# Kernel tuning notes

Hardware: AMD Instinct MI355X
Metric: run time of the kernel (lower is better)

The kernel has to match this reference:

```python
import jax, jax.numpy as jnp
import numpy as np

N_NODES = 100000
N_EDGES = 1600000
IN_C, HID, OUT_C = 128, 128, 64
BN_EPS = 1e-5


def gcn_conv(x, W, b, src, dst):
    # PyG GCNConv(normalize=False): linear first, then sum-aggregate over edges
    m = x @ W                                   # [N, out_dim]
    agg = jax.ops.segment_sum(m[src], dst, num_segments=N_NODES)  # scatter-add by dst
    return agg + b


def batch_norm(h, gamma, beta):
    mu = jnp.mean(h, axis=0)
    var = jnp.var(h, axis=0)
    return (h - mu) * jax.lax.rsqrt(var + BN_EPS) * gamma + beta


def setup_inputs() -> dict:
    key = jax.random.key(0)
    ks = jax.random.split(key, 8)
    x = jax.random.normal(ks[0], (N_NODES, IN_C), dtype=jnp.float32)
    edge_src = jax.random.randint(ks[1], (N_EDGES,), 0, N_NODES, dtype=jnp.int32)
    edge_dst = jnp.sort(jax.random.randint(ks[2], (N_EDGES,), 0, N_NODES, dtype=jnp.int32))
    def glorot(k, shape):
        lim = float(np.sqrt(6.0 / (shape[0] + shape[1])))
        return jax.random.uniform(k, shape, jnp.float32, -lim, lim)
    return {
        "x": x, "edge_src": edge_src, "edge_dst": edge_dst,
        "W0": glorot(ks[3], (IN_C, HID)), "b0": jnp.zeros((HID,), jnp.float32),
        "W1": glorot(ks[4], (HID, HID)), "b1": jnp.zeros((HID,), jnp.float32),
        "W2": glorot(ks[5], (HID, OUT_C)), "b2": jnp.zeros((OUT_C,), jnp.float32),
        "g0": jnp.ones((HID,), jnp.float32), "be0": jnp.zeros((HID,), jnp.float32),
        "g1": jnp.ones((HID,), jnp.float32), "be1": jnp.zeros((HID,), jnp.float32),
    }


def reference(x, edge_src, edge_dst, W0, b0, W1, b1, W2, b2, g0, be0, g1, be1):
    # layer 0: conv -> BN -> residual (dims match: 128==128) -> ReLU (dropout p=0)
    h = gcn_conv(x, W0, b0, edge_src, edge_dst)
    h = batch_norm(h, g0, be0)
    h = h + x  # residual, in_channels == hidden_channels
    x1 = jax.nn.relu(h)
    # layer 1
    h = gcn_conv(x1, W1, b1, edge_src, edge_dst)
    h = batch_norm(h, g1, be1)
    h = h + x1
    x2 = jax.nn.relu(h)
    # final layer: conv only
    return gcn_conv(x2, W2, b2, edge_src, edge_dst)
```

## Files before the change

kernel.cpp:

```cpp
#include <hip/hip_runtime.h>

#define BN_EPS 1e-5f

typedef __attribute__((ext_vector_type(8))) short bf16x8;
typedef __attribute__((ext_vector_type(4))) float f32x4;

__device__ __forceinline__ short f2bf(float f) {
    union { float f; unsigned u; } v; v.f = f;
    unsigned r = (v.u + 0x7fffu + ((v.u >> 16) & 1u)) >> 16;
    return (short)r;
}
__device__ __forceinline__ float bflo(unsigned d) {
    union { unsigned u; float f; } v; v.u = d << 16; return v.f;
}
__device__ __forceinline__ float bfhi(unsigned d) {
    union { unsigned u; float f; } v; v.u = d & 0xffff0000u; return v.f;
}

__global__ __launch_bounds__(256) void build_off_k(const int* __restrict__ dst,
                                                   int* __restrict__ off, int E, int N) {
    int i = blockIdx.x * 256 + threadIdx.x;
    if (i > E) return;
    int cur  = (i < E) ? dst[i] : N;
    int prev = (i == 0) ? -1 : dst[i - 1];
    for (int n = prev + 1; n <= cur; ++n) off[n] = i;
}

__global__ void zero_k(float* p, int n) {
    int i = blockIdx.x * blockDim.x + threadIdx.x;
    if (i < n) p[i] = 0.f;
}

__global__ __launch_bounds__(256) void wtrans_k(const float* __restrict__ W,
                                                short* __restrict__ Wt, int K, int C) {
    int i = blockIdx.x * 256 + threadIdx.x;
    if (i >= K * C) return;
    int c = i / K, k = i % K;
    Wt[i] = f2bf(W[k * C + c]);
}

template <int OUTC, int MODE>
__global__ __launch_bounds__(256) void mgemm_k(const float* __restrict__ X,
                                               const short* __restrict__ Wt,
                                               short* __restrict__ M,
                                               const float* __restrict__ ss,
                                               const void* __restrict__ Rp,
                                               short* __restrict__ X1, int N) {
    constexpr int NR = OUTC / 16;
    __shared__ short sW[OUTC][136];

    const int tid = threadIdx.x;
    for (int q = tid; q < OUTC * 16; q += 256) {
        int r = q >> 4, s = q & 15;
        *(int4*)&sW[r][s * 8] = ((const int4*)Wt)[q];
    }
    __syncthreads();

    const int wave = tid >> 6, lane = tid & 63;
    const int lr = lane & 15, lg = lane >> 4;
    const int row0 = blockIdx.x * 128 + wave * 32;

    f32x4 acc[2][NR];
    #pragma unroll
    for (int m = 0; m < 2; ++m)
        #pragma unroll
        for (int n = 0; n < NR; ++n) acc[m][n] = (f32x4){0.f, 0.f, 0.f, 0.f};

    #pragma unroll
    for (int kk = 0; kk < 4; ++kk) {
        bf16x8 a[2];
        const int ch0 = kk * 32 + lg * 8;
        #pragma unroll
        for (int m = 0; m < 2; ++m) {
            int row = row0 + m * 16 + lr;
            float v[8] = {0.f, 0.f, 0.f, 0.f, 0.f, 0.f, 0.f, 0.f};
            if (row < N) {
                const float4* p = (const float4*)&X[(size_t)row * 128 + ch0];
                float4 h0 = p[0], h1 = p[1];
                v[0] = h0.x; v[1] = h0.y; v[2] = h0.z; v[3] = h0.w;
                v[4] = h1.x; v[5] = h1.y; v[6] = h1.z; v[7] = h1.w;
                if constexpr (MODE != 0) {
                    float4 sc0 = *(const float4*)&ss[ch0];
                    float4 sc1 = *(const float4*)&ss[ch0 + 4];
                    float4 sh0 = *(const float4*)&ss[128 + ch0];
                    float4 sh1 = *(const float4*)&ss[128 + ch0 + 4];
                    float sc[8] = {sc0.x, sc0.y, sc0.z, sc0.w, sc1.x, sc1.y, sc1.z, sc1.w};
                    float sh[8] = {sh0.x, sh0.y, sh0.z, sh0.w, sh1.x, sh1.y, sh1.z, sh1.w};
                    float r[8];
                    if constexpr (MODE == 1) {
                        const float4* rp = (const float4*)((const float*)Rp + (size_t)row * 128 + ch0);
                        float4 r0 = rp[0], r1 = rp[1];
                        r[0] = r0.x; r[1] = r0.y; r[2] = r0.z; r[3] = r0.w;
                        r[4] = r1.x; r[5] = r1.y; r[6] = r1.z; r[7] = r1.w;
                    } else {
                        int4 rb = *(const int4*)((const short*)Rp + (size_t)row * 128 + ch0);
                        r[0] = bflo(rb.x); r[1] = bfhi(rb.x);
                        r[2] = bflo(rb.y); r[3] = bfhi(rb.y);
                        r[4] = bflo(rb.z); r[5] = bfhi(rb.z);
                        r[6] = bflo(rb.w); r[7] = bfhi(rb.w);
                    }
                    #pragma unroll
                    for (int k = 0; k < 8; ++k)
                        v[k] = fmaxf(fmaf(v[k], sc[k], sh[k]) + r[k], 0.f);
                }
            }
            #pragma unroll
            for (int k = 0; k < 8; ++k) a[m][k] = f2bf(v[k]);
            if constexpr (MODE == 1) {
                if (row < N) *(bf16x8*)&X1[(size_t)row * 128 + ch0] = a[m];
            }
        }
        #pragma unroll
        for (int n = 0; n < NR; ++n) {
            bf16x8 b = *(const bf16x8*)&sW[n * 16 + lr][kk * 32 + lg * 8];
            acc[0][n] = __builtin_amdgcn_mfma_f32_16x16x32_bf16(a[0], b, acc[0][n], 0, 0, 0);
            acc[1][n] = __builtin_amdgcn_mfma_f32_16x16x32_bf16(a[1], b, acc[1][n], 0, 0, 0);
        }
    }

    #pragma unroll
    for (int m = 0; m < 2; ++m)
        #pragma unroll
        for (int r = 0; r < 4; ++r) {
            int row = row0 + m * 16 + lg * 4 + r;
            if (row < N) {
                #pragma unroll
                for (int n = 0; n < NR; ++n)
                    M[(size_t)row * OUTC + n * 16 + lr] = f2bf(acc[m][n][r]);
            }
        }
}

template <int C, bool STATS>
__global__ __launch_bounds__(256) void agg_k(const short* __restrict__ M,
                                             const int* __restrict__ src,
                                             const int* __restrict__ off,
                                             const float* __restrict__ bias,
                                             float* __restrict__ H,
                                             float* __restrict__ stats, int N) {
    constexpr int T = C / 8;
    constexpr int G = 64 / T;
    const int wave = threadIdx.x >> 6, lane = threadIdx.x & 63;
    const int g = lane / T, t = lane % T;
    const uint4* __restrict__ Mq = (const uint4*)M;

    float sum[8], sq[8];
    if constexpr (STATS) {
        #pragma unroll
        for (int k = 0; k < 8; ++k) { sum[k] = 0.f; sq[k] = 0.f; }
    }

    for (int node = blockIdx.x * 4 + wave; node < N; node += gridDim.x * 4) {
        const int e0 = off[node], e1 = off[node + 1];
        float acc[8];
        #pragma unroll
        for (int k = 0; k < 8; ++k) acc[k] = 0.f;

        for (int base = e0; base < e1; base += 64) {
            int cnt = e1 - base; if (cnt > 64) cnt = 64;
            int s = (base + lane < e1) ? src[base + lane] : 0;
            int ngrp = (cnt + G - 1) / G;
            for (int j = 0; j < ngrp; j += 2) {
                int i0 = j * G + g, i1 = i0 + G;
                int s0 = __shfl(s, i0), s1 = __shfl(s, i1 & 63);
                uint4 d0 = make_uint4(0u, 0u, 0u, 0u), d1 = d0;
                if (i0 < cnt) d0 = Mq[(size_t)s0 * T + t];
                if (i1 < cnt) d1 = Mq[(size_t)s1 * T + t];
                acc[0] += bflo(d0.x); acc[1] += bfhi(d0.x);
                acc[2] += bflo(d0.y); acc[3] += bfhi(d0.y);
                acc[4] += bflo(d0.z); acc[5] += bfhi(d0.z);
                acc[6] += bflo(d0.w); acc[7] += bfhi(d0.w);
                acc[0] += bflo(d1.x); acc[1] += bfhi(d1.x);
                acc[2] += bflo(d1.y); acc[3] += bfhi(d1.y);
                acc[4] += bflo(d1.z); acc[5] += bfhi(d1.z);
                acc[6] += bflo(d1.w); acc[7] += bfhi(d1.w);
            }
        }
        #pragma unroll
        for (int dlt = T; dlt < 64; dlt <<= 1)
            #pragma unroll
            for (int k = 0; k < 8; ++k) acc[k] += __shfl_xor(acc[k], dlt);

        float h[8];
        #pragma unroll
        for (int k = 0; k < 8; ++k) h[k] = acc[k] + bias[t * 8 + k];
        if (g == 0) {
            *(float4*)&H[(size_t)node * C + t * 8]     = make_float4(h[0], h[1], h[2], h[3]);
            *(float4*)&H[(size_t)node * C + t * 8 + 4] = make_float4(h[4], h[5], h[6], h[7]);
            if constexpr (STATS) {
                #pragma unroll
                for (int k = 0; k < 8; ++k) {
                    sum[k] += h[k]; sq[k] = fmaf(h[k], h[k], sq[k]);
                }
            }
        }
    }

    if constexpr (STATS) {
        __shared__ float sL[4 * 256];
        if (g == 0) {
            #pragma unroll
            for (int k = 0; k < 8; ++k) {
                sL[wave * 256 + t * 8 + k]       = sum[k];
                sL[wave * 256 + 128 + t * 8 + k] = sq[k];
            }
        }
        __syncthreads();
        int tid = threadIdx.x;
        float v = sL[tid] + sL[256 + tid] + sL[512 + tid] + sL[768 + tid];
        atomicAdd(&stats[tid], v);
    }
}

__global__ void bnfin_k(const float* __restrict__ stats, const float* __restrict__ gamma,
                        const float* __restrict__ beta, float* __restrict__ ss, float invN) {
    int c = threadIdx.x;
    float mu  = stats[c] * invN;
    float var = fmaf(-mu, mu, stats[128 + c] * invN);
    float sc  = gamma[c] * rsqrtf(var + BN_EPS);
    ss[c]       = sc;
    ss[128 + c] = fmaf(-mu, sc, beta[c]);
}

extern "C" void kernel_launch(void* const* d_in, const int* in_sizes, int n_in,
                              void* d_out, int out_size, void* d_ws, size_t ws_size,
                              hipStream_t stream) {
    const float* x   = (const float*)d_in[0];
    const int*   src = (const int*)d_in[1];
    const int*   dst = (const int*)d_in[2];
    const float* W0  = (const float*)d_in[3];
    const float* b0  = (const float*)d_in[4];
    const float* W1  = (const float*)d_in[5];
    const float* b1  = (const float*)d_in[6];
    const float* W2  = (const float*)d_in[7];
    const float* b2  = (const float*)d_in[8];
    const float* g0  = (const float*)d_in[9];
    const float* be0 = (const float*)d_in[10];
    const float* g1  = (const float*)d_in[11];
    const float* be1 = (const float*)d_in[12];
    float* out = (float*)d_out;

    const int N = in_sizes[0] / 128;
    const int E = in_sizes[1];

    char*  ws   = (char*)d_ws;
    size_t bufB = (size_t)N * 128 * sizeof(float);
    short* Mb = (short*)(ws);
    float* H  = (float*)(ws + bufB);
    short* X1 = (short*)(ws + 2 * bufB);
    size_t p  = 2 * bufB + bufB / 2;
    p = (p + 255) & ~(size_t)255;
    int*   off = (int*)(ws + p);
    p += ((size_t)(N + 1) * sizeof(int) + 255) & ~(size_t)255;
    float* stats0 = (float*)(ws + p); p += 1024;
    float* stats1 = (float*)(ws + p); p += 1024;
    float* ss0    = (float*)(ws + p); p += 1024;
    float* ss1    = (float*)(ws + p); p += 1024;
    short* Wt0    = (short*)(ws + p); p += 128 * 128 * 2;
    short* Wt1    = (short*)(ws + p); p += 128 * 128 * 2;
    short* Wt2    = (short*)(ws + p); p += 128 * 64 * 2;

    const dim3 blk(256);
    const int gGemm = (N + 127) / 128;
    const int gAgg  = 1024;
    const float invN = 1.f / (float)N;

    zero_k<<<2, blk, 0, stream>>>(stats0, 512);
    wtrans_k<<<64, blk, 0, stream>>>(W0, Wt0, 128, 128);
    wtrans_k<<<64, blk, 0, stream>>>(W1, Wt1, 128, 128);
    wtrans_k<<<32, blk, 0, stream>>>(W2, Wt2, 128, 64);
    build_off_k<<<(E + 256) / 256, blk, 0, stream>>>(dst, off, E, N);

    mgemm_k<128, 0><<<gGemm, blk, 0, stream>>>(x, Wt0, Mb, nullptr, nullptr, nullptr, N);
    agg_k<128, true><<<gAgg, blk, 0, stream>>>(Mb, src, off, b0, H, stats0, N);
    bnfin_k<<<1, 128, 0, stream>>>(stats0, g0, be0, ss0, invN);

    mgemm_k<128, 1><<<gGemm, blk, 0, stream>>>(H, Wt1, Mb, ss0, x, X1, N);
    agg_k<128, true><<<gAgg, blk, 0, stream>>>(Mb, src, off, b1, H, stats1, N);
    bnfin_k<<<1, 128, 0, stream>>>(stats1, g1, be1, ss1, invN);

    mgemm_k<64, 2><<<gGemm, blk, 0, stream>>>(H, Wt2, Mb, ss1, X1, nullptr, N);
    agg_k<64, false><<<gAgg, blk, 0, stream>>>(Mb, src, off, b2, out, stats0, N);
}
```

Before: 322.5 us.

## Store intermediate aggregation output in bf16, unroll gather by four, enlarge agg grid

The aggregation kernels for layers 0 and 1 now write the pre-BN hidden H as bf16 instead of fp32, and the following GEMMs read bf16. This halves the H write and read traffic. BN statistics are still accumulated from the fp32 values. The gather loop now issues four independent row loads per iteration instead of two, for more memory-level parallelism, and the aggregation grid grows from 1024 to 4096 blocks. The cost is extra bf16 rounding of H before normalization and the residual, which adds a small accuracy risk.

```diff
diff --git a/kernel.cpp b/kernel.cpp
--- a/kernel.cpp
+++ b/kernel.cpp
@@ -40,7 +40,7 @@
 }
 
 template <int OUTC, int MODE>
-__global__ __launch_bounds__(256) void mgemm_k(const float* __restrict__ X,
+__global__ __launch_bounds__(256) void mgemm_k(const void* __restrict__ Xp,
                                                const short* __restrict__ Wt,
                                                short* __restrict__ M,
                                                const float* __restrict__ ss,
@@ -75,11 +75,17 @@
             int row = row0 + m * 16 + lr;
             float v[8] = {0.f, 0.f, 0.f, 0.f, 0.f, 0.f, 0.f, 0.f};
             if (row < N) {
-                const float4* p = (const float4*)&X[(size_t)row * 128 + ch0];
-                float4 h0 = p[0], h1 = p[1];
-                v[0] = h0.x; v[1] = h0.y; v[2] = h0.z; v[3] = h0.w;
-                v[4] = h1.x; v[5] = h1.y; v[6] = h1.z; v[7] = h1.w;
-                if constexpr (MODE != 0) {
+                if constexpr (MODE == 0) {
+                    const float4* p = (const float4*)((const float*)Xp + (size_t)row * 128 + ch0);
+                    float4 h0 = p[0], h1 = p[1];
+                    v[0] = h0.x; v[1] = h0.y; v[2] = h0.z; v[3] = h0.w;
+                    v[4] = h1.x; v[5] = h1.y; v[6] = h1.z; v[7] = h1.w;
+                } else {
+                    int4 hb = *(const int4*)((const short*)Xp + (size_t)row * 128 + ch0);
+                    v[0] = bflo(hb.x); v[1] = bfhi(hb.x);
+                    v[2] = bflo(hb.y); v[3] = bfhi(hb.y);
+                    v[4] = bflo(hb.z); v[5] = bfhi(hb.z);
+                    v[6] = bflo(hb.w); v[7] = bfhi(hb.w);
                     float4 sc0 = *(const float4*)&ss[ch0];
                     float4 sc1 = *(const float4*)&ss[ch0 + 4];
                     float4 sh0 = *(const float4*)&ss[128 + ch0];
@@ -131,12 +137,12 @@
         }
 }
 
-template <int C, bool STATS>
+template <int C, bool STATS, bool OUTBF>
 __global__ __launch_bounds__(256) void agg_k(const short* __restrict__ M,
                                              const int* __restrict__ src,
                                              const int* __restrict__ off,
                                              const float* __restrict__ bias,
-                                             float* __restrict__ H,
+                                             void* __restrict__ Hp,
                                              float* __restrict__ stats, int N) {
     constexpr int T = C / 8;
     constexpr int G = 64 / T;
@@ -160,20 +166,23 @@
             int cnt = e1 - base; if (cnt > 64) cnt = 64;
             int s = (base + lane < e1) ? src[base + lane] : 0;
             int ngrp = (cnt + G - 1) / G;
-            for (int j = 0; j < ngrp; j += 2) {
-                int i0 = j * G + g, i1 = i0 + G;
-                int s0 = __shfl(s, i0), s1 = __shfl(s, i1 & 63);
-                uint4 d0 = make_uint4(0u, 0u, 0u, 0u), d1 = d0;
+            for (int j = 0; j < ngrp; j += 4) {
+                int i0 = j * G + g, i1 = i0 + G, i2 = i0 + 2 * G, i3 = i0 + 3 * G;
+                int s0 = __shfl(s, i0 & 63), s1 = __shfl(s, i1 & 63);
+                int s2 = __shfl(s, i2 & 63), s3 = __shfl(s, i3 & 63);
+                uint4 d0 = make_uint4(0u,0u,0u,0u), d1 = d0, d2 = d0, d3 = d0;
                 if (i0 < cnt) d0 = Mq[(size_t)s0 * T + t];
                 if (i1 < cnt) d1 = Mq[(size_t)s1 * T + t];
-                acc[0] += bflo(d0.x); acc[1] += bfhi(d0.x);
-                acc[2] += bflo(d0.y); acc[3] += bfhi(d0.y);
-                acc[4] += bflo(d0.z); acc[5] += bfhi(d0.z);
-                acc[6] += bflo(d0.w); acc[7] += bfhi(d0.w);
-                acc[0] += bflo(d1.x); acc[1] += bfhi(d1.x);
-                acc[2] += bflo(d1.y); acc[3] += bfhi(d1.y);
-                acc[4] += bflo(d1.z); acc[5] += bfhi(d1.z);
-                acc[6] += bflo(d1.w); acc[7] += bfhi(d1.w);
+                if (i2 < cnt) d2 = Mq[(size_t)s2 * T + t];
+                if (i3 < cnt) d3 = Mq[(size_t)s3 * T + t];
+                acc[0] += bflo(d0.x) + bflo(d1.x); acc[1] += bfhi(d0.x) + bfhi(d1.x);
+                acc[2] += bflo(d0.y) + bflo(d1.y); acc[3] += bfhi(d0.y) + bfhi(d1.y);
+                acc[4] += bflo(d0.z) + bflo(d1.z); acc[5] += bfhi(d0.z) + bfhi(d1.z);
+                acc[6] += bflo(d0.w) + bflo(d1.w); acc[7] += bfhi(d0.w) + bfhi(d1.w);
+                acc[0] += bflo(d2.x) + bflo(d3.x); acc[1] += bfhi(d2.x) + bfhi(d3.x);
+                acc[2] += bflo(d2.y) + bflo(d3.y); acc[3] += bfhi(d2.y) + bfhi(d3.y);
+                acc[4] += bflo(d2.z) + bflo(d3.z); acc[5] += bfhi(d2.z) + bfhi(d3.z);
+                acc[6] += bflo(d2.w) + bflo(d3.w); acc[7] += bfhi(d2.w) + bfhi(d3.w);
             }
         }
         #pragma unroll
@@ -181,12 +190,19 @@
             #pragma unroll
             for (int k = 0; k < 8; ++k) acc[k] += __shfl_xor(acc[k], dlt);
 
-        float h[8];
-        #pragma unroll
-        for (int k = 0; k < 8; ++k) h[k] = acc[k] + bias[t * 8 + k];
         if (g == 0) {
-            *(float4*)&H[(size_t)node * C + t * 8]     = make_float4(h[0], h[1], h[2], h[3]);
-            *(float4*)&H[(size_t)node * C + t * 8 + 4] = make_float4(h[4], h[5], h[6], h[7]);
+            float h[8];
+            #pragma unroll
+            for (int k = 0; k < 8; ++k) h[k] = acc[k] + bias[t * 8 + k];
+            if constexpr (OUTBF) {
+                bf16x8 hv;
+                #pragma unroll
+                for (int k = 0; k < 8; ++k) hv[k] = f2bf(h[k]);
+                *(bf16x8*)((short*)Hp + (size_t)node * C + t * 8) = hv;
+            } else {
+                *(float4*)((float*)Hp + (size_t)node * C + t * 8)     = make_float4(h[0], h[1], h[2], h[3]);
+                *(float4*)((float*)Hp + (size_t)node * C + t * 8 + 4) = make_float4(h[4], h[5], h[6], h[7]);
+            }
             if constexpr (STATS) {
                 #pragma unroll
                 for (int k = 0; k < 8; ++k) {
@@ -244,11 +260,11 @@
     const int E = in_sizes[1];
 
     char*  ws   = (char*)d_ws;
-    size_t bufB = (size_t)N * 128 * sizeof(float);
+    size_t bufH = (size_t)N * 128 * sizeof(short);
     short* Mb = (short*)(ws);
-    float* H  = (float*)(ws + bufB);
-    short* X1 = (short*)(ws + 2 * bufB);
-    size_t p  = 2 * bufB + bufB / 2;
+    short* Hb = (short*)(ws + bufH);
+    short* X1 = (short*)(ws + 2 * bufH);
+    size_t p  = 3 * bufH;
     p = (p + 255) & ~(size_t)255;
     int*   off = (int*)(ws + p);
     p += ((size_t)(N + 1) * sizeof(int) + 255) & ~(size_t)255;
@@ -262,7 +278,7 @@
 
     const dim3 blk(256);
     const int gGemm = (N + 127) / 128;
-    const int gAgg  = 1024;
+    const int gAgg  = 4096;
     const float invN = 1.f / (float)N;
 
     zero_k<<<2, blk, 0, stream>>>(stats0, 512);
@@ -272,13 +288,13 @@
     build_off_k<<<(E + 256) / 256, blk, 0, stream>>>(dst, off, E, N);
 
     mgemm_k<128, 0><<<gGemm, blk, 0, stream>>>(x, Wt0, Mb, nullptr, nullptr, nullptr, N);
-    agg_k<128, true><<<gAgg, blk, 0, stream>>>(Mb, src, off, b0, H, stats0, N);
+    agg_k<128, true, true><<<gAgg, blk, 0, stream>>>(Mb, src, off, b0, Hb, stats0, N);
     bnfin_k<<<1, 128, 0, stream>>>(stats0, g0, be0, ss0, invN);
 
-    mgemm_k<128, 1><<<gGemm, blk, 0, stream>>>(H, Wt1, Mb, ss0, x, X1, N);
-    agg_k<128, true><<<gAgg, blk, 0, stream>>>(Mb, src, off, b1, H, stats1, N);
+    mgemm_k<128, 1><<<gGemm, blk, 0, stream>>>(Hb, Wt1, Mb, ss0, x, X1, N);
+    agg_k<128, true, true><<<gAgg, blk, 0, stream>>>(Mb, src, off, b1, Hb, stats1, N);
     bnfin_k<<<1, 128, 0, stream>>>(stats1, g1, be1, ss1, invN);
 
-    mgemm_k<64, 2><<<gGemm, blk, 0, stream>>>(H, Wt2, Mb, ss1, X1, nullptr, N);
-    agg_k<64, false><<<gAgg, blk, 0, stream>>>(Mb, src, off, b2, out, stats0, N);
-}
+    mgemm_k<64, 2><<<gGemm, blk, 0, stream>>>(Hb, Wt2, Mb, ss1, X1, nullptr, N);
+    agg_k<64, false, false><<<gAgg, blk, 0, stream>>>(Mb, src, off, b2, out, stats0, N);
+}
```

Measured after the change: 380.3 us. 1.18x slower.
